# Performance work log

Hardware: AMD Instinct MI355X
Metric: run time of the kernel (lower is better)

Reference implementation:

```python
import jax, jax.numpy as jnp
import numpy as np

N = 50000   # nodes
E = 500000  # edges
H = 128     # hidden_dim


def setup_inputs() -> dict:
    key = jax.random.key(0)
    ks = jax.random.split(key, 8)
    w = lambda k, shp: jax.random.normal(k, shp, jnp.float32) * 0.02
    return {
        "edge_idx": jax.random.randint(ks[0], (E, 2), 0, N, dtype=jnp.int32),
        "node_feats": jax.random.normal(ks[1], (N, H), jnp.float32),
        "edge_feats": jax.random.normal(ks[2], (E, H), jnp.float32),
        # edge MLP params: Linear(3H,H) -> ReLU -> Linear(H,H) -> LayerNorm(H)
        "We1": w(ks[3], (3 * H, H)), "be1": jnp.zeros((H,), jnp.float32),
        "We2": w(ks[4], (H, H)),     "be2": jnp.zeros((H,), jnp.float32),
        "ge": jnp.ones((H,), jnp.float32), "bge": jnp.zeros((H,), jnp.float32),
        # node MLP params: Linear(2H,H) -> ReLU -> Linear(H,H) -> LayerNorm(H)
        "Wn1": w(ks[5], (2 * H, H)), "bn1": jnp.zeros((H,), jnp.float32),
        "Wn2": w(ks[6], (H, H)),     "bn2": jnp.zeros((H,), jnp.float32),
        "gn": jnp.ones((H,), jnp.float32), "bgn": jnp.zeros((H,), jnp.float32),
    }


def layer_norm(x, g, b, eps=1e-5):
    m = jnp.mean(x, axis=-1, keepdims=True)
    v = jnp.var(x, axis=-1, keepdims=True)
    return (x - m) * jax.lax.rsqrt(v + eps) * g + b


def reference(edge_idx, node_feats, edge_feats,
              We1, be1, We2, be2, ge, bge,
              Wn1, bn1, Wn2, bn2, gn, bgn):
    senders = edge_idx[:, 0]
    receivers = edge_idx[:, 1]
    # edge update: gather endpoints, concat with edge feats, MLP + LN
    e_in = jnp.concatenate([node_feats[senders], node_feats[receivers], edge_feats], axis=-1)  # [E, 3H]
    edge_update = layer_norm(jax.nn.relu(e_in @ We1 + be1) @ We2 + be2, ge, bge)               # [E, H]
    # faithful to source: scatter-add of edge_feats (NOT edge_update) into receivers
    acc = jax.ops.segment_sum(edge_feats, receivers, num_segments=node_feats.shape[0])          # [N, H]
    n_in = jnp.concatenate([node_feats, acc], axis=-1)                                          # [N, 2H]
    node_update = layer_norm(jax.nn.relu(n_in @ Wn1 + bn1) @ Wn2 + bn2, gn, bgn)                # [N, H]
    return node_feats + node_update, edge_feats + edge_update
```

## Files before the change

kernel.cpp:

```cpp
#include <hip/hip_runtime.h>
#include <hip/hip_bf16.h>

#define DI __device__ __forceinline__

typedef __attribute__((ext_vector_type(8))) short short8;
typedef __attribute__((ext_vector_type(4))) short short4v;
typedef __attribute__((ext_vector_type(4))) float floatx4;

constexpr int NN = 50000;
constexpr int NE = 500000;
constexpr int H  = 128;
constexpr int NB1 = (NN + 255) / 256;

constexpr size_t OFF_BF   = 262144;
constexpr size_t OFF_PS   = 327680;
constexpr size_t OFF_PR   = 13127680;
constexpr size_t OFF_CNT  = 25927680;
constexpr size_t OFF_TMP  = 26127680;
constexpr size_t OFF_RS   = 26327680;
constexpr size_t OFF_CUR  = 26527680;
constexpr size_t OFF_BSUM = 26727680;
constexpr size_t OFF_CSR  = 26728704;

constexpr int WF_TOTAL = 131072;
constexpr int BIASF_FLOATS = 8*2048;

DI short f2bf(float f){ __bf16 b = (__bf16)f; return __builtin_bit_cast(short, b); }
DI float bf2f(short s){ return __builtin_bit_cast(float, ((unsigned)(unsigned short)s) << 16); }

__global__ __launch_bounds__(256) void zero_cnt_kernel(int* __restrict__ cnt){
  int i = blockIdx.x*256 + threadIdx.x;
  if (i < NN) cnt[i] = 0;
}

__global__ __launch_bounds__(256) void prep_kernel(
    const float* __restrict__ We1, const float* __restrict__ We2,
    const float* __restrict__ Wn1, const float* __restrict__ Wn2,
    const float* __restrict__ be1, const float* __restrict__ be2,
    const float* __restrict__ ge,  const float* __restrict__ bge,
    const float* __restrict__ bn1, const float* __restrict__ bn2,
    const float* __restrict__ gn,  const float* __restrict__ bgn,
    short* __restrict__ wf, float* __restrict__ bf)
{
  int t = blockIdx.x*256 + threadIdx.x;
  if (t < WF_TOTAL) {
    int blk = t >> 14, u = t & 16383;
    int j = u & 7, l = (u>>3)&63, nt = (u>>9)&7, ks = u>>12;
    const float* src; int roff; bool blayout = false;
    switch (blk) {
      case 0: src = We1; roff = 0;   break;
      case 1: src = We1; roff = 128; break;
      case 2: src = We1; roff = 256; break;
      case 3: src = We2; roff = 0;   break;
      case 4: src = Wn1; roff = 0;   break;
      case 5: src = Wn1; roff = 128; break;
      case 6: src = Wn2; roff = 0;   break;
      default: src = We2; roff = 0; blayout = true; break;
    }
    int row = blayout ? (32*ks + 16*(j>>2) + 4*(l>>4) + (j&3))
                      : (roff + 32*ks + 8*(l>>4) + j);
    int col = 16*nt + (l&15);
    wf[t] = f2bf(src[row*H + col]);
  } else if (t < WF_TOTAL + BIASF_FLOATS) {
    int tb = t - WF_TOTAL;
    int arr = tb >> 11, u = tb & 2047;
    int r = u&3, l = (u>>2)&63, mt = u>>8;
    int feat = 16*mt + 4*(l>>4) + r;
    const float* s;
    switch (arr) {
      case 0: s = be1; break; case 1: s = be2; break;
      case 2: s = ge;  break; case 3: s = bge; break;
      case 4: s = bn1; break; case 5: s = bn2; break;
      case 6: s = gn;  break; default: s = bgn; break;
    }
    bf[tb] = s[feat];
  }
}

__global__ __launch_bounds__(256) void hist_kernel(const int* __restrict__ ei, int* __restrict__ cnt){
  int e = blockIdx.x*256 + threadIdx.x;
  if (e < NE) atomicAdd(&cnt[ei[2*e+1]], 1);
}

__global__ __launch_bounds__(256) void scan1_kernel(const int* __restrict__ cnt,
                                                    int* __restrict__ tmp, int* __restrict__ blocksum){
  __shared__ int s[256];
  int t = threadIdx.x, i = blockIdx.x*256 + t;
  int v = (i < NN) ? cnt[i] : 0;
  s[t] = v; __syncthreads();
#pragma unroll
  for (int o=1; o<256; o<<=1){
    int u = (t >= o) ? s[t-o] : 0;
    __syncthreads();
    s[t] += u;
    __syncthreads();
  }
  if (i < NN) tmp[i] = s[t];
  if (t == 255) blocksum[blockIdx.x] = s[255];
}

__global__ __launch_bounds__(256) void scan2_kernel(int* __restrict__ blocksum){
  __shared__ int s[256];
  int t = threadIdx.x;
  int v = (t < NB1) ? blocksum[t] : 0;
  s[t] = v; __syncthreads();
#pragma unroll
  for (int o=1; o<256; o<<=1){
    int u = (t >= o) ? s[t-o] : 0;
    __syncthreads();
    s[t] += u;
    __syncthreads();
  }
  if (t < NB1) blocksum[t] = s[t] - v;
}

__global__ __launch_bounds__(256) void scan3_kernel(const int* __restrict__ cnt, const int* __restrict__ tmp,
                                                    const int* __restrict__ blocksum,
                                                    int* __restrict__ rowstart, int* __restrict__ cursor){
  int i = blockIdx.x*256 + threadIdx.x;
  if (i < NN){
    int rs = tmp[i] - cnt[i] + blocksum[blockIdx.x];
    rowstart[i] = rs; cursor[i] = rs;
  }
}

__global__ __launch_bounds__(256) void scatter_kernel(const int* __restrict__ ei,
                                                      int* __restrict__ cursor, int* __restrict__ csr){
  int e = blockIdx.x*256 + threadIdx.x;
  if (e < NE){
    int r = ei[2*e+1];
    int p = atomicAdd(&cursor[r], 1);
    csr[p] = e;
  }
}

__global__ __launch_bounds__(256) void segsum_kernel(const int* __restrict__ csr,
                                                     const int* __restrict__ rowstart,
                                                     const int* __restrict__ cnt,
                                                     const float* __restrict__ edge_feats,
                                                     float* __restrict__ acc){
  int tid = threadIdx.x;
  int w = tid>>6, l = tid&63;
  int hh = l>>5, q = l&31;
  int n = blockIdx.x*8 + w*2 + hh;
  if (n >= NN) return;
  int start = rowstart[n], deg = cnt[n];
  floatx4 s = floatx4{0.f,0.f,0.f,0.f};
  int k = 0;
  for (; k+4 <= deg; k += 4){
    int e0 = csr[start+k],   e1 = csr[start+k+1];
    int e2 = csr[start+k+2], e3 = csr[start+k+3];
    floatx4 v0 = *(const floatx4*)(edge_feats + (size_t)e0*H + 4*q);
    floatx4 v1 = *(const floatx4*)(edge_feats + (size_t)e1*H + 4*q);
    floatx4 v2 = *(const floatx4*)(edge_feats + (size_t)e2*H + 4*q);
    floatx4 v3 = *(const floatx4*)(edge_feats + (size_t)e3*H + 4*q);
    s += v0; s += v1; s += v2; s += v3;
  }
  for (; k < deg; ++k){
    int e = csr[start+k];
    s += *(const floatx4*)(edge_feats + (size_t)e*H + 4*q);
  }
  *(floatx4*)(acc + (size_t)n*H + 4*q) = s;
}

__global__ __launch_bounds__(256) void pproj_kernel(
    const float* __restrict__ node_feats,
    const short* __restrict__ wsf, const short* __restrict__ wrf,
    const float* __restrict__ b1f,
    short* __restrict__ Ps, short* __restrict__ Pr)
{
  const int tid = threadIdx.x;
  const int w = tid>>6, l = tid&63, g = l>>4, lo = l&15;
  int row = blockIdx.x*64 + w*16 + lo;
  bool valid = row < NN;
  int rowc = valid ? row : (NN-1);
  const float* sp = node_feats + (size_t)rowc*H;

  short8 ein[4];
#pragma unroll
  for (int ks=0; ks<4; ++ks){
    const int koff = ks*32 + g*8;
    floatx4 f0 = *(const floatx4*)(sp + koff);
    floatx4 f1 = *(const floatx4*)(sp + koff + 4);
    ein[ks][0]=f2bf(f0[0]); ein[ks][1]=f2bf(f0[1]); ein[ks][2]=f2bf(f0[2]); ein[ks][3]=f2bf(f0[3]);
    ein[ks][4]=f2bf(f1[0]); ein[ks][5]=f2bf(f1[1]); ein[ks][6]=f2bf(f1[2]); ein[ks][7]=f2bf(f1[3]);
  }

  floatx4 as[8], ar[8];
#pragma unroll
  for (int mt=0; mt<8; ++mt){ as[mt] = floatx4{0,0,0,0}; ar[mt] = floatx4{0,0,0,0}; }
#pragma unroll
  for (int ks=0; ks<4; ++ks){
#pragma unroll
    for (int mt=0; mt<8; ++mt){
      short8 wv = *(const short8*)(wsf + ((ks*8+mt)*64 + l)*8);
      as[mt] = __builtin_amdgcn_mfma_f32_16x16x32_bf16(wv, ein[ks], as[mt], 0,0,0);
      short8 wv2 = *(const short8*)(wrf + ((ks*8+mt)*64 + l)*8);
      ar[mt] = __builtin_amdgcn_mfma_f32_16x16x32_bf16(wv2, ein[ks], ar[mt], 0,0,0);
    }
  }

  if (valid){
    short* ps = Ps + (size_t)rowc*H + g*32;
    short* pr = Pr + (size_t)rowc*H + g*32;
#pragma unroll
    for (int mt=0; mt<8; ++mt){
      floatx4 bv = *(const floatx4*)(b1f + (mt*64+l)*4);
      short4v vs, vr;
#pragma unroll
      for (int r=0; r<4; ++r){ vs[r] = f2bf(as[mt][r] + bv[r]); vr[r] = f2bf(ar[mt][r]); }
      *(short4v*)(ps + mt*4) = vs;
      *(short4v*)(pr + mt*4) = vr;
    }
  }
}

template<int R>
__global__ __launch_bounds__(512) void edge_kernel(
    const int* __restrict__ edge_idx,
    const float* __restrict__ edge_feats,
    const short* __restrict__ Ps, const short* __restrict__ Pr,
    const short* __restrict__ wef, const short* __restrict__ w2fB,
    const float* __restrict__ b2f,
    const float* __restrict__ gf,  const float* __restrict__ bgf,
    float* __restrict__ out_edge)
{
  extern __shared__ short smem[];
  short* wA = smem;
  short* wB = smem + 16384;
  const int tid = threadIdx.x;
  const int w = tid>>6, l = tid&63, g = l>>4, lo = l&15;

  int rowc[R]; bool valid[R]; int2 se[R];
#pragma unroll
  for (int b=0; b<R; ++b){
    int row = blockIdx.x*(8*16*R) + w*(16*R) + b*16 + lo;
    valid[b] = row < NE;
    rowc[b]  = valid[b] ? row : (NE-1);
    se[b] = *(const int2*)(edge_idx + 2*rowc[b]);
  }

#pragma unroll
  for (int rnd=0; rnd<4; ++rnd){
    int o = (rnd*512 + tid)*8;
    *(short8*)(wA + o) = *(const short8*)(wef  + o);
    *(short8*)(wB + o) = *(const short8*)(w2fB + o);
  }

  short8 vs[4], vr[4];
  {
    const short* ps = Ps + (size_t)se[0].x*H + g*32;
    const short* pr = Pr + (size_t)se[0].y*H + g*32;
#pragma unroll
    for (int m2=0; m2<4; ++m2){
      vs[m2] = *(const short8*)(ps + m2*8);
      vr[m2] = *(const short8*)(pr + m2*8);
    }
  }
  floatx4 ef[8];
  {
    const float* sp = edge_feats + (size_t)rowc[0]*H;
#pragma unroll
    for (int ks=0; ks<4; ++ks){
      ef[2*ks]   = *(const floatx4*)(sp + ks*32 + g*8);
      ef[2*ks+1] = *(const floatx4*)(sp + ks*32 + g*8 + 4);
    }
  }
  __syncthreads();

#pragma unroll
  for (int b=0; b<R; ++b){
    short8 ein[4];
#pragma unroll
    for (int ks=0; ks<4; ++ks){
      ein[ks][0]=f2bf(ef[2*ks][0]);   ein[ks][1]=f2bf(ef[2*ks][1]);
      ein[ks][2]=f2bf(ef[2*ks][2]);   ein[ks][3]=f2bf(ef[2*ks][3]);
      ein[ks][4]=f2bf(ef[2*ks+1][0]); ein[ks][5]=f2bf(ef[2*ks+1][1]);
      ein[ks][6]=f2bf(ef[2*ks+1][2]); ein[ks][7]=f2bf(ef[2*ks+1][3]);
    }

    if (b+1 < R){
      const float* sp = edge_feats + (size_t)rowc[b+1]*H;
#pragma unroll
      for (int ks=0; ks<4; ++ks){
        ef[2*ks]   = *(const floatx4*)(sp + ks*32 + g*8);
        ef[2*ks+1] = *(const floatx4*)(sp + ks*32 + g*8 + 4);
      }
    }

    floatx4 acc[8];
#pragma unroll
    for (int mt=0; mt<8; ++mt) acc[mt] = floatx4{0.f,0.f,0.f,0.f};
#pragma unroll
    for (int ks=0; ks<4; ++ks){
#pragma unroll
      for (int mt=0; mt<8; ++mt){
        short8 wv = *(const short8*)(wA + ((ks*8+mt)*64 + l)*8);
        acc[mt] = __builtin_amdgcn_mfma_f32_16x16x32_bf16(wv, ein[ks], acc[mt], 0,0,0);
      }
    }

#pragma unroll
    for (int m2=0; m2<4; ++m2)
#pragma unroll
      for (int r=0; r<4; ++r){
        acc[2*m2][r]   += bf2f(vs[m2][r])   + bf2f(vr[m2][r]);
        acc[2*m2+1][r] += bf2f(vs[m2][4+r]) + bf2f(vr[m2][4+r]);
      }

    if (b+1 < R){
      const short* ps = Ps + (size_t)se[b+1].x*H + g*32;
      const short* pr = Pr + (size_t)se[b+1].y*H + g*32;
#pragma unroll
      for (int m2=0; m2<4; ++m2){
        vs[m2] = *(const short8*)(ps + m2*8);
        vr[m2] = *(const short8*)(pr + m2*8);
      }
    }

    short8 hb[4];
#pragma unroll
    for (int s=0; s<4; ++s){
#pragma unroll
      for (int r=0; r<4; ++r){
        float v0 = acc[2*s][r];
        float v1 = acc[2*s+1][r];
        hb[s][r]   = f2bf(v0 > 0.f ? v0 : 0.f);
        hb[s][4+r] = f2bf(v1 > 0.f ? v1 : 0.f);
      }
    }

#pragma unroll
    for (int mt=0; mt<8; ++mt) acc[mt] = *(const floatx4*)(b2f + (mt*64+l)*4);
#pragma unroll
    for (int s=0; s<4; ++s){
#pragma unroll
      for (int mt=0; mt<8; ++mt){
        short8 wv = *(const short8*)(wB + ((s*8+mt)*64 + l)*8);
        acc[mt] = __builtin_amdgcn_mfma_f32_16x16x32_bf16(wv, hb[s], acc[mt], 0,0,0);
      }
    }

    float sum = 0.f, ssq = 0.f;
#pragma unroll
    for (int mt=0; mt<8; ++mt)
#pragma unroll
      for (int r=0; r<4; ++r){ float v = acc[mt][r]; sum += v; ssq += v*v; }
    sum += __shfl_xor(sum, 16); ssq += __shfl_xor(ssq, 16);
    sum += __shfl_xor(sum, 32); ssq += __shfl_xor(ssq, 32);
    const float mean = sum * (1.f/H);
    const float var  = ssq * (1.f/H) - mean*mean;
    const float rs   = rsqrtf(var + 1e-5f);

    const float* resid = edge_feats + (size_t)rowc[b]*H;
    float* outp = out_edge + (size_t)rowc[b]*H;
#pragma unroll
    for (int mt=0; mt<8; ++mt){
      floatx4 gv  = *(const floatx4*)(gf  + (mt*64+l)*4);
      floatx4 bgv = *(const floatx4*)(bgf + (mt*64+l)*4);
      floatx4 efr = *(const floatx4*)(resid + mt*16 + g*4);
      floatx4 o;
#pragma unroll
      for (int r=0; r<4; ++r) o[r] = efr[r] + (acc[mt][r]-mean)*rs*gv[r] + bgv[r];
      if (valid[b]) *(floatx4*)(outp + mt*16 + g*4) = o;
    }
  }
}

__global__ __launch_bounds__(256) void node_kernel(
    const float* __restrict__ node_feats,
    const short* __restrict__ w1f, const short* __restrict__ w2f,
    const float* __restrict__ b1f, const float* __restrict__ b2f,
    const float* __restrict__ gf,  const float* __restrict__ bgf,
    float* __restrict__ out_node)
{
  __shared__ short lds_h[4*2048];
  const int tid = threadIdx.x;
  const int w = tid>>6, l = tid&63, g = l>>4, lo = l&15;
  short* ldsw = lds_h + w*2048;

  int row = blockIdx.x*64 + w*16 + lo;
  bool valid = row < NN;
  int rowc = valid ? row : (NN-1);
  const float* sp0 = node_feats + (size_t)rowc*H;
  const float* sp1 = out_node   + (size_t)rowc*H;

  floatx4 acc1[8];
#pragma unroll
  for (int mt=0; mt<8; ++mt) acc1[mt] = *(const floatx4*)(b1f + (mt*64+l)*4);

#pragma unroll
  for (int ks=0; ks<8; ++ks){
    const float* sp = (ks<4) ? sp0 : sp1;
    const int koff = (ks&3)*32 + g*8;
    floatx4 f0 = *(const floatx4*)(sp + koff);
    floatx4 f1 = *(const floatx4*)(sp + koff + 4);
    short8 ein;
    ein[0]=f2bf(f0[0]); ein[1]=f2bf(f0[1]); ein[2]=f2bf(f0[2]); ein[3]=f2bf(f0[3]);
    ein[4]=f2bf(f1[0]); ein[5]=f2bf(f1[1]); ein[6]=f2bf(f1[2]); ein[7]=f2bf(f1[3]);
#pragma unroll
    for (int mt=0; mt<8; ++mt){
      short8 wv = *(const short8*)(w1f + ((ks*8+mt)*64 + l)*8);
      acc1[mt] = __builtin_amdgcn_mfma_f32_16x16x32_bf16(wv, ein, acc1[mt], 0,0,0);
    }
  }

#pragma unroll
  for (int mt=0; mt<8; ++mt){
    short4v hv;
#pragma unroll
    for (int r=0; r<4; ++r){
      float v = acc1[mt][r];
      hv[r] = f2bf(v > 0.f ? v : 0.f);
    }
    int off = (lo*256 + mt*32 + g*8) ^ ((lo&7)<<4);
    *(short4v*)((char*)ldsw + off) = hv;
  }

  floatx4 acc2[8];
#pragma unroll
  for (int mt=0; mt<8; ++mt) acc2[mt] = *(const floatx4*)(b2f + (mt*64+l)*4);

#pragma unroll
  for (int s=0; s<4; ++s){
    int roff = (lo*256 + s*64 + g*16) ^ ((lo&7)<<4);
    short8 hb = *(const short8*)((char*)ldsw + roff);
#pragma unroll
    for (int mt=0; mt<8; ++mt){
      short8 wv = *(const short8*)(w2f + ((s*8+mt)*64 + l)*8);
      acc2[mt] = __builtin_amdgcn_mfma_f32_16x16x32_bf16(wv, hb, acc2[mt], 0,0,0);
    }
  }

  float sum = 0.f, ssq = 0.f;
#pragma unroll
  for (int mt=0; mt<8; ++mt)
#pragma unroll
    for (int r=0; r<4; ++r){ float v = acc2[mt][r]; sum += v; ssq += v*v; }
  sum += __shfl_xor(sum, 16); ssq += __shfl_xor(ssq, 16);
  sum += __shfl_xor(sum, 32); ssq += __shfl_xor(ssq, 32);
  const float mean = sum * (1.f/H);
  const float var  = ssq * (1.f/H) - mean*mean;
  const float rs   = rsqrtf(var + 1e-5f);

#pragma unroll
  for (int mt=0; mt<8; ++mt){
    floatx4 gv  = *(const floatx4*)(gf  + (mt*64+l)*4);
    floatx4 bgv = *(const floatx4*)(bgf + (mt*64+l)*4);
    floatx4 nf  = *(const floatx4*)(node_feats + (size_t)rowc*H + mt*16 + g*4);
    floatx4 o;
#pragma unroll
    for (int r=0; r<4; ++r) o[r] = nf[r] + (acc2[mt][r]-mean)*rs*gv[r] + bgv[r];
    if (valid) *(floatx4*)(out_node + (size_t)rowc*H + mt*16 + g*4) = o;
  }
}

extern "C" void kernel_launch(void* const* d_in, const int* in_sizes, int n_in,
                              void* d_out, int out_size, void* d_ws, size_t ws_size,
                              hipStream_t stream)
{
  const int*   edge_idx   = (const int*)  d_in[0];
  const float* node_feats = (const float*)d_in[1];
  const float* edge_feats = (const float*)d_in[2];
  const float* We1=(const float*)d_in[3];  const float* be1=(const float*)d_in[4];
  const float* We2=(const float*)d_in[5];  const float* be2=(const float*)d_in[6];
  const float* ge =(const float*)d_in[7];  const float* bge=(const float*)d_in[8];
  const float* Wn1=(const float*)d_in[9];  const float* bn1=(const float*)d_in[10];
  const float* Wn2=(const float*)d_in[11]; const float* bn2=(const float*)d_in[12];
  const float* gn =(const float*)d_in[13]; const float* bgn=(const float*)d_in[14];

  float* out_node = (float*)d_out;
  float* out_edge = out_node + (size_t)NN*H;

  char* ws = (char*)d_ws;
  short* wf      = (short*)ws;
  float* bf      = (float*)(ws + OFF_BF);
  short* Ps      = (short*)(ws + OFF_PS);
  short* Pr      = (short*)(ws + OFF_PR);
  int* cnt       = (int*)(ws + OFF_CNT);
  int* tmp       = (int*)(ws + OFF_TMP);
  int* rowstart  = (int*)(ws + OFF_RS);
  int* cursor    = (int*)(ws + OFF_CUR);
  int* blocksum  = (int*)(ws + OFF_BSUM);
  int* csr       = (int*)(ws + OFF_CSR);

  short* wsf  = wf;
  short* wrf  = wf + 16384;
  short* wef  = wf + 32768;
  short* wn1f = wf + 65536;
  short* wn2f = wf + 98304;
  short* w2fB = wf + 114688;
  float* b1f  = bf;         float* b2f  = bf + 2048;
  float* gef  = bf + 4096;  float* bgef = bf + 6144;
  float* bn1f = bf + 8192;  float* bn2f = bf + 10240;
  float* gnf  = bf + 12288; float* bgnf = bf + 14336;

  zero_cnt_kernel<<<NB1, 256, 0, stream>>>(cnt);
  prep_kernel<<<(WF_TOTAL + BIASF_FLOATS + 255)/256, 256, 0, stream>>>(
      We1, We2, Wn1, Wn2, be1, be2, ge, bge, bn1, bn2, gn, bgn, wf, bf);

  hist_kernel<<<(NE+255)/256, 256, 0, stream>>>(edge_idx, cnt);
  scan1_kernel<<<NB1, 256, 0, stream>>>(cnt, tmp, blocksum);
  scan2_kernel<<<1, 256, 0, stream>>>(blocksum);
  scan3_kernel<<<NB1, 256, 0, stream>>>(cnt, tmp, blocksum, rowstart, cursor);
  scatter_kernel<<<(NE+255)/256, 256, 0, stream>>>(edge_idx, cursor, csr);

  pproj_kernel<<<(NN+63)/64, 256, 0, stream>>>(node_feats, wsf, wrf, b1f, Ps, Pr);

  edge_kernel<2><<<(NE + 255)/256, 512, 65536, stream>>>(
      edge_idx, edge_feats, Ps, Pr, wef, w2fB, b2f, gef, bgef, out_edge);

  segsum_kernel<<<(NN+7)/8, 256, 0, stream>>>(csr, rowstart, cnt, edge_feats, out_node);

  node_kernel<<<(NN+63)/64, 256, 0, stream>>>(
      node_feats, wn1f, wn2f, bn1f, bn2f, gnf, bgnf, out_node);
}
```

Before: 358.5 us.

## Fold count zeroing into prep, merge scan passes, double-buffer gathers with R=4

Zeroing of the histogram counts moves into the prep kernel, and the single-block scan2 is removed: each scan3 block now sums the preceding block totals itself with a wavefront reduction. Together these drop two kernel launches. The edge kernel now handles 4 row tiles per wave (half as many blocks) and double-buffers the gathered Ps/Pr rows two iterations ahead, giving the gathers more time to land before use. The cost is more registers per thread, which may lower occupancy, and redundant prefix summation across the scan3 blocks.

```diff
diff --git a/kernel.cpp b/kernel.cpp
--- a/kernel.cpp
+++ b/kernel.cpp
@@ -24,14 +24,10 @@
 
 constexpr int WF_TOTAL = 131072;
 constexpr int BIASF_FLOATS = 8*2048;
+constexpr int PREP_TOTAL = WF_TOTAL + BIASF_FLOATS + NN;
 
 DI short f2bf(float f){ __bf16 b = (__bf16)f; return __builtin_bit_cast(short, b); }
 DI float bf2f(short s){ return __builtin_bit_cast(float, ((unsigned)(unsigned short)s) << 16); }
-
-__global__ __launch_bounds__(256) void zero_cnt_kernel(int* __restrict__ cnt){
-  int i = blockIdx.x*256 + threadIdx.x;
-  if (i < NN) cnt[i] = 0;
-}
 
 __global__ __launch_bounds__(256) void prep_kernel(
     const float* __restrict__ We1, const float* __restrict__ We2,
@@ -40,7 +36,7 @@
     const float* __restrict__ ge,  const float* __restrict__ bge,
     const float* __restrict__ bn1, const float* __restrict__ bn2,
     const float* __restrict__ gn,  const float* __restrict__ bgn,
-    short* __restrict__ wf, float* __restrict__ bf)
+    short* __restrict__ wf, float* __restrict__ bf, int* __restrict__ cnt)
 {
   int t = blockIdx.x*256 + threadIdx.x;
   if (t < WF_TOTAL) {
@@ -74,6 +70,8 @@
       case 6: s = gn;  break; default: s = bgn; break;
     }
     bf[tb] = s[feat];
+  } else if (t < PREP_TOTAL) {
+    cnt[t - WF_TOTAL - BIASF_FLOATS] = 0;
   }
 }
 
@@ -99,27 +97,22 @@
   if (t == 255) blocksum[blockIdx.x] = s[255];
 }
 
-__global__ __launch_bounds__(256) void scan2_kernel(int* __restrict__ blocksum){
-  __shared__ int s[256];
-  int t = threadIdx.x;
-  int v = (t < NB1) ? blocksum[t] : 0;
-  s[t] = v; __syncthreads();
-#pragma unroll
-  for (int o=1; o<256; o<<=1){
-    int u = (t >= o) ? s[t-o] : 0;
-    __syncthreads();
-    s[t] += u;
-    __syncthreads();
-  }
-  if (t < NB1) blocksum[t] = s[t] - v;
-}
-
 __global__ __launch_bounds__(256) void scan3_kernel(const int* __restrict__ cnt, const int* __restrict__ tmp,
                                                     const int* __restrict__ blocksum,
                                                     int* __restrict__ rowstart, int* __restrict__ cursor){
-  int i = blockIdx.x*256 + threadIdx.x;
+  __shared__ int pfx;
+  int t = threadIdx.x, bid = blockIdx.x;
+  if (t < 64){
+    int p = 0;
+    for (int k = t; k < bid; k += 64) p += blocksum[k];
+#pragma unroll
+    for (int o=32; o>0; o>>=1) p += __shfl_down(p, o);
+    if (t == 0) pfx = p;
+  }
+  __syncthreads();
+  int i = bid*256 + t;
   if (i < NN){
-    int rs = tmp[i] - cnt[i] + blocksum[blockIdx.x];
+    int rs = tmp[i] - cnt[i] + pfx;
     rowstart[i] = rs; cursor[i] = rs;
   }
 }
@@ -247,14 +240,23 @@
     *(short8*)(wB + o) = *(const short8*)(w2fB + o);
   }
 
-  short8 vs[4], vr[4];
+  short8 vs0[4], vr0[4], vs1[4], vr1[4];
   {
     const short* ps = Ps + (size_t)se[0].x*H + g*32;
     const short* pr = Pr + (size_t)se[0].y*H + g*32;
 #pragma unroll
     for (int m2=0; m2<4; ++m2){
-      vs[m2] = *(const short8*)(ps + m2*8);
-      vr[m2] = *(const short8*)(pr + m2*8);
+      vs0[m2] = *(const short8*)(ps + m2*8);
+      vr0[m2] = *(const short8*)(pr + m2*8);
+    }
+  }
+  if (R > 1){
+    const short* ps = Ps + (size_t)se[1].x*H + g*32;
+    const short* pr = Pr + (size_t)se[1].y*H + g*32;
+#pragma unroll
+    for (int m2=0; m2<4; ++m2){
+      vs1[m2] = *(const short8*)(ps + m2*8);
+      vr1[m2] = *(const short8*)(pr + m2*8);
     }
   }
   floatx4 ef[8];
@@ -300,22 +302,22 @@
       }
     }
 
-#pragma unroll
-    for (int m2=0; m2<4; ++m2)
-#pragma unroll
-      for (int r=0; r<4; ++r){
-        acc[2*m2][r]   += bf2f(vs[m2][r])   + bf2f(vr[m2][r]);
-        acc[2*m2+1][r] += bf2f(vs[m2][4+r]) + bf2f(vr[m2][4+r]);
-      }
-
-    if (b+1 < R){
-      const short* ps = Ps + (size_t)se[b+1].x*H + g*32;
-      const short* pr = Pr + (size_t)se[b+1].y*H + g*32;
-#pragma unroll
-      for (int m2=0; m2<4; ++m2){
-        vs[m2] = *(const short8*)(ps + m2*8);
-        vr[m2] = *(const short8*)(pr + m2*8);
-      }
+    if ((b & 1) == 0){
+#pragma unroll
+      for (int m2=0; m2<4; ++m2)
+#pragma unroll
+        for (int r=0; r<4; ++r){
+          acc[2*m2][r]   += bf2f(vs0[m2][r])   + bf2f(vr0[m2][r]);
+          acc[2*m2+1][r] += bf2f(vs0[m2][4+r]) + bf2f(vr0[m2][4+r]);
+        }
+    } else {
+#pragma unroll
+      for (int m2=0; m2<4; ++m2)
+#pragma unroll
+        for (int r=0; r<4; ++r){
+          acc[2*m2][r]   += bf2f(vs1[m2][r])   + bf2f(vr1[m2][r]);
+          acc[2*m2+1][r] += bf2f(vs1[m2][4+r]) + bf2f(vr1[m2][4+r]);
+        }
     }
 
     short8 hb[4];
@@ -363,6 +365,24 @@
 #pragma unroll
       for (int r=0; r<4; ++r) o[r] = efr[r] + (acc[mt][r]-mean)*rs*gv[r] + bgv[r];
       if (valid[b]) *(floatx4*)(outp + mt*16 + g*4) = o;
+    }
+
+    if (b+2 < R){
+      const short* ps = Ps + (size_t)se[b+2].x*H + g*32;
+      const short* pr = Pr + (size_t)se[b+2].y*H + g*32;
+      if ((b & 1) == 0){
+#pragma unroll
+        for (int m2=0; m2<4; ++m2){
+          vs0[m2] = *(const short8*)(ps + m2*8);
+          vr0[m2] = *(const short8*)(pr + m2*8);
+        }
+      } else {
+#pragma unroll
+        for (int m2=0; m2<4; ++m2){
+          vs1[m2] = *(const short8*)(ps + m2*8);
+          vr1[m2] = *(const short8*)(pr + m2*8);
+        }
+      }
     }
   }
 }
@@ -495,19 +515,17 @@
   float* bn1f = bf + 8192;  float* bn2f = bf + 10240;
   float* gnf  = bf + 12288; float* bgnf = bf + 14336;
 
-  zero_cnt_kernel<<<NB1, 256, 0, stream>>>(cnt);
-  prep_kernel<<<(WF_TOTAL + BIASF_FLOATS + 255)/256, 256, 0, stream>>>(
-      We1, We2, Wn1, Wn2, be1, be2, ge, bge, bn1, bn2, gn, bgn, wf, bf);
+  prep_kernel<<<(PREP_TOTAL + 255)/256, 256, 0, stream>>>(
+      We1, We2, Wn1, Wn2, be1, be2, ge, bge, bn1, bn2, gn, bgn, wf, bf, cnt);
 
   hist_kernel<<<(NE+255)/256, 256, 0, stream>>>(edge_idx, cnt);
   scan1_kernel<<<NB1, 256, 0, stream>>>(cnt, tmp, blocksum);
-  scan2_kernel<<<1, 256, 0, stream>>>(blocksum);
   scan3_kernel<<<NB1, 256, 0, stream>>>(cnt, tmp, blocksum, rowstart, cursor);
   scatter_kernel<<<(NE+255)/256, 256, 0, stream>>>(edge_idx, cursor, csr);
 
   pproj_kernel<<<(NN+63)/64, 256, 0, stream>>>(node_feats, wsf, wrf, b1f, Ps, Pr);
 
-  edge_kernel<2><<<(NE + 255)/256, 512, 65536, stream>>>(
+  edge_kernel<4><<<(NE + 511)/512, 512, 65536, stream>>>(
       edge_idx, edge_feats, Ps, Pr, wef, w2fB, b2f, gef, bgef, out_edge);
 
   segsum_kernel<<<(NN+7)/8, 256, 0, stream>>>(csr, rowstart, cnt, edge_feats, out_node);
```

Measured after the change: 362.4 us. No clear change (+1.1%).
